# Kernel optimization log

Measured on AMD Instinct MI355X. Metric: run time of the kernel, lower is better.

The kernel has to match this reference:

```python
import jax, jax.numpy as jnp
import numpy as np

# Model dims
T0 = 2048      # tokens (batch*seq flattened)
D = 2048       # hidden_size
E = 256        # n_routed_experts
K = 8          # num_experts_per_tok
G = 8          # expert groups
EG = 32        # experts per group
R = 64         # tucker rank
I = 1408       # moe_intermediate_size


def setup_inputs() -> dict:
    key = jax.random.key(0)
    ks = jax.random.split(key, 12)
    f = lambda k, s: jax.random.normal(k, s, dtype=jnp.float32) * 0.02
    return {
        "hidden_states": jax.random.normal(ks[0], (T0, D), dtype=jnp.float32),
        "w_gate": f(ks[1], (D, E)),
        # Tucker factors per group: shared in-factor A, per-expert core C, shared out-factor B
        "A_gate": f(ks[2], (G, D, R)), "C_gate": f(ks[3], (G, EG, R, R)), "B_gate": f(ks[4], (G, R, I)),
        "A_up":   f(ks[5], (G, D, R)), "C_up":   f(ks[6], (G, EG, R, R)), "B_up":   f(ks[7], (G, R, I)),
        "A_down": f(ks[8], (G, I, R)), "C_down": f(ks[9], (G, EG, R, R)), "B_down": f(ks[10], (G, R, D)),
    }


def _tucker(x, A, C, B, inner):
    # x: [T, d_in], A: [d_in, R], C: [EG, R, R] gathered per-token, B: [R, d_out]
    h1 = x @ A                                    # [T, R]
    h2 = jnp.einsum('tr,trs->ts', h1, C[inner])   # per-token expert core
    return h2 @ B                                 # [T, d_out]


def reference(hidden_states, w_gate, A_gate, C_gate, B_gate,
              A_up, C_up, B_up, A_down, C_down, B_down):
    # Router: softmax in fp32, top-k, renormalize
    logits = hidden_states @ w_gate                              # [T0, E]
    probs = jax.nn.softmax(logits.astype(jnp.float32), axis=-1)
    rw, sel = jax.lax.top_k(probs, K)                            # [T0, K]
    rw = (rw / rw.sum(axis=-1, keepdims=True)).astype(hidden_states.dtype)

    idx = sel.reshape(-1)          # [T0*K] expert ids of dispatched rows
    gid = idx // EG                # group id
    inner = idx % EG               # expert within group
    x = jnp.repeat(hidden_states, K, axis=0)   # repeat_interleave dispatch [T0*K, D]

    out = jnp.zeros_like(x)
    for g in range(G):             # static loop over 8 structurally distinct groups
        m = (gid == g)[:, None]
        xg = jnp.where(m, x, 0.0)  # masked dispatch (zeros flow to zero through the MLP)
        go = _tucker(xg, A_gate[g], C_gate[g], B_gate[g], inner)
        uo = _tucker(xg, A_up[g],   C_up[g],   B_up[g],   inner)
        inter = jax.nn.silu(go) * uo
        do = _tucker(inter, A_down[g], C_down[g], B_down[g], inner)
        out = out + jnp.where(m, do, 0.0)

    # weighted combine
    return (out.reshape(T0, K, D) * rw[..., None]).sum(axis=1)
```

## Files before the change

### kernel.cpp

```cpp
#include <hip/hip_runtime.h>
#include <math.h>

constexpr int T0n = 2048;
constexpr int Dn  = 2048;
constexpr int En  = 256;
constexpr int Gn  = 8;
constexpr int EGn = 32;
constexpr int Rn  = 64;
constexpr int In  = 1408;

constexpr int NROWS = T0n * 8;
constexpr int SEGCAP = NROWS;
constexpr int KSPLIT = 8;

typedef __attribute__((ext_vector_type(8))) short s8v;
typedef __attribute__((ext_vector_type(4))) float f4v;
#define MFMA16(a, b, c) __builtin_amdgcn_mfma_f32_16x16x32_bf16(a, b, c, 0, 0, 0)

__device__ __forceinline__ unsigned short f2bf(float x) {
  unsigned int u = __float_as_uint(x);
  unsigned int r = (u + 0x7FFFu + ((u >> 16) & 1u)) >> 16;
  return (unsigned short)r;
}

struct TD { const float* src; unsigned short* dst; int rows, cols, nbx, per_batch, base; };
struct TD9 { TD t[9]; };

__global__ __launch_bounds__(256) void k_tcvt9(TD9 D) {
  __shared__ float tbuf[32][33];
  int id = blockIdx.x;
  int ti = 0;
#pragma unroll
  for (int i = 1; i < 9; ++i) ti = (id >= D.t[i].base) ? i : ti;
  TD d = D.t[ti];
  int local = id - d.base;
  int bz = local / d.per_batch;
  int rem = local - bz * d.per_batch;
  int by = rem / d.nbx;
  int bx = rem - by * d.nbx;

  size_t boff = (size_t)bz * d.rows * d.cols;
  const float* src = d.src + boff;
  unsigned short* dst = d.dst + boff;
  int c0 = bx * 32, r0 = by * 32;
  int tx = threadIdx.x & 31, ty = threadIdx.x >> 5;
  for (int i = ty; i < 32; i += 8)
    tbuf[i][tx] = src[(size_t)(r0 + i) * d.cols + c0 + tx];
  __syncthreads();
  for (int i = ty; i < 32; i += 8)
    dst[(size_t)(c0 + i) * d.rows + r0 + tx] = f2bf(tbuf[tx][i]);
}

__global__ __launch_bounds__(256) void k_router_part(
    const float* __restrict__ A, const float* __restrict__ B,
    double* __restrict__ part) {
  __shared__ float As[32][68];
  __shared__ float Bs[32][68];
  const int m0 = blockIdx.y * 64, n0 = blockIdx.x * 64;
  const int kc = blockIdx.z;
  const int kbeg = kc * (Dn / KSPLIT);
  const int tid = threadIdx.x;
  const int ty = tid >> 4, tx = tid & 15;
  const int lm = tid & 63, lk8 = (tid >> 6) * 8;
  const int br = tid >> 3, bc = (tid & 7) * 8;

  double acc[4][4] = {};

  for (int k0 = kbeg; k0 < kbeg + Dn / KSPLIT; k0 += 32) {
    float4 a0 = *(const float4*)&A[(size_t)(m0 + lm) * Dn + k0 + lk8];
    float4 a1 = *(const float4*)&A[(size_t)(m0 + lm) * Dn + k0 + lk8 + 4];
    As[lk8 + 0][lm] = a0.x; As[lk8 + 1][lm] = a0.y;
    As[lk8 + 2][lm] = a0.z; As[lk8 + 3][lm] = a0.w;
    As[lk8 + 4][lm] = a1.x; As[lk8 + 5][lm] = a1.y;
    As[lk8 + 6][lm] = a1.z; As[lk8 + 7][lm] = a1.w;
    *(float4*)&Bs[br][bc]     = *(const float4*)&B[(size_t)(k0 + br) * En + n0 + bc];
    *(float4*)&Bs[br][bc + 4] = *(const float4*)&B[(size_t)(k0 + br) * En + n0 + bc + 4];
    __syncthreads();
#pragma unroll
    for (int kk = 0; kk < 32; ++kk) {
      float4 af = *(const float4*)&As[kk][ty * 4];
      float4 bf = *(const float4*)&Bs[kk][tx * 4];
      double a[4] = {(double)af.x, (double)af.y, (double)af.z, (double)af.w};
      double b[4] = {(double)bf.x, (double)bf.y, (double)bf.z, (double)bf.w};
#pragma unroll
      for (int i = 0; i < 4; ++i)
#pragma unroll
        for (int j = 0; j < 4; ++j)
          acc[i][j] += a[i] * b[j];
    }
    __syncthreads();
  }
  double* prow = part + (size_t)kc * T0n * En;
#pragma unroll
  for (int i = 0; i < 4; ++i) {
    int row = m0 + ty * 4 + i;
#pragma unroll
    for (int j2 = 0; j2 < 2; ++j2) {
      double2 dv;
      dv.x = acc[i][j2 * 2 + 0];
      dv.y = acc[i][j2 * 2 + 1];
      *(double2*)&prow[(size_t)row * En + n0 + tx * 4 + j2 * 2] = dv;
    }
  }
}

__global__ __launch_bounds__(256) void k_topk(
    const double* __restrict__ part, int* __restrict__ sel,
    float* __restrict__ rw, int* __restrict__ cnt_e) {
  const int wid = threadIdx.x >> 6, ln = threadIdx.x & 63;
  const int t = blockIdx.x * 4 + wid;

  double v[4];
#pragma unroll
  for (int j = 0; j < 4; ++j) {
    double s = 0.0;
#pragma unroll
    for (int kc = 0; kc < KSPLIT; ++kc)
      s += part[((size_t)kc * T0n + t) * En + ln + 64 * j];
    v[j] = s;
  }

  float topv[8];
  int topi[8];
#pragma unroll
  for (int k = 0; k < 8; ++k) {
    double bv = v[0]; int bi = ln;
#pragma unroll
    for (int j = 1; j < 4; ++j) {
      int cand = ln + 64 * j;
      if (v[j] > bv || (v[j] == bv && cand < bi)) { bv = v[j]; bi = cand; }
    }
#pragma unroll
    for (int off = 32; off > 0; off >>= 1) {
      double ov = __shfl_xor(bv, off);
      int oi = __shfl_xor(bi, off);
      if (ov > bv || (ov == bv && oi < bi)) { bv = ov; bi = oi; }
    }
    topv[k] = (float)bv; topi[k] = bi;
    if ((bi & 63) == ln) v[bi >> 6] = -1e300;
  }

  if (ln < 8) {
    float m = topv[0];
    float ssum = 0.f;
#pragma unroll
    for (int k = 0; k < 8; ++k) ssum += expf(topv[k] - m);
    rw[t * 8 + ln] = expf(topv[ln] - m) / ssum;
    sel[t * 8 + ln] = topi[ln];
    atomicAdd(&cnt_e[topi[ln]], 1);
  }
}

__global__ __launch_bounds__(256) void k_scan(
    const int* __restrict__ cnt_e, int* __restrict__ off_e,
    int* __restrict__ cur_e, int* __restrict__ grp_n) {
  __shared__ int c[256];
  int tid = threadIdx.x;
  c[tid] = cnt_e[tid];
  __syncthreads();
  int g = tid >> 5, ei = tid & 31;
  int run = 0;
  for (int i = 0; i < ei; ++i) run += c[(g << 5) + i];
  off_e[tid] = g * SEGCAP + run;
  cur_e[tid] = g * SEGCAP + run;
  if (ei == 31) grp_n[g] = run + c[tid];
}

__global__ void k_scatter(const int* __restrict__ sel, int* __restrict__ cur_e,
                          int* __restrict__ rseg) {
  int i = blockIdx.x * 256 + threadIdx.x;
  int e = sel[i];
  int pos = atomicAdd(&cur_e[e], 1);
  rseg[pos] = i;
}

__global__ __launch_bounds__(512) void k_h1_mfma(
    const float* __restrict__ H,
    const unsigned short* __restrict__ AgT, const unsigned short* __restrict__ AuT,
    unsigned short* __restrict__ h1gb, unsigned short* __restrict__ h1ub) {
  const int t0 = blockIdx.x * 64;
  const int g = blockIdx.y;
  const unsigned short* Wg = AgT + (size_t)g * Rn * Dn;
  const unsigned short* Wu = AuT + (size_t)g * Rn * Dn;

  __shared__ unsigned short As[64 * 72];
  __shared__ unsigned short Bg_l[64 * 72];
  __shared__ unsigned short Bu_l[64 * 72];
  const int tid = threadIdx.x;
  const int w = tid >> 6, ln = tid & 63;
  const int path = w >> 2, ws = w & 3;
  const int quad = ln >> 4, lane16 = ln & 15;
  const int j = tid >> 3, q = (tid & 7) * 8;

  f4v S[4] = {};

  for (int k0 = 0; k0 < Dn; k0 += 64) {
    {
      float4 v0 = *(const float4*)&H[(size_t)(t0 + j) * Dn + k0 + q];
      float4 v1 = *(const float4*)&H[(size_t)(t0 + j) * Dn + k0 + q + 4];
      ushort4 o0, o1;
      o0.x = f2bf(v0.x); o0.y = f2bf(v0.y); o0.z = f2bf(v0.z); o0.w = f2bf(v0.w);
      o1.x = f2bf(v1.x); o1.y = f2bf(v1.y); o1.z = f2bf(v1.z); o1.w = f2bf(v1.w);
      *(ushort4*)&As[j * 72 + q] = o0;
      *(ushort4*)&As[j * 72 + q + 4] = o1;
      *(uint4*)&Bg_l[j * 72 + q] = *(const uint4*)&Wg[(size_t)j * Dn + k0 + q];
      *(uint4*)&Bu_l[j * 72 + q] = *(const uint4*)&Wu[(size_t)j * Dn + k0 + q];
    }
    __syncthreads();
    const unsigned short* Bl = path ? Bu_l : Bg_l;
#pragma unroll
    for (int kk = 0; kk < 2; ++kk) {
      s8v a = *(const s8v*)&As[(ws * 16 + lane16) * 72 + kk * 32 + quad * 8];
#pragma unroll
      for (int nt = 0; nt < 4; ++nt) {
        s8v b = *(const s8v*)&Bl[(nt * 16 + lane16) * 72 + kk * 32 + quad * 8];
        S[nt] = MFMA16(a, b, S[nt]);
      }
    }
    __syncthreads();
  }
  unsigned short* out = path ? h1ub : h1gb;
#pragma unroll
  for (int nt = 0; nt < 4; ++nt)
#pragma unroll
    for (int r = 0; r < 4; ++r) {
      int row = t0 + ws * 16 + quad * 4 + r;
      int col = g * 64 + nt * 16 + lane16;
      out[(size_t)row * (Gn * Rn) + col] = f2bf(S[nt][r]);
    }
}

__global__ __launch_bounds__(512) void k_core_gu(
    const unsigned short* __restrict__ h1gb, const unsigned short* __restrict__ h1ub,
    const unsigned short* __restrict__ CgT, const unsigned short* __restrict__ CuT,
    const int* __restrict__ rseg, const int* __restrict__ off_e,
    const int* __restrict__ cnt_e,
    unsigned short* __restrict__ h2gb, unsigned short* __restrict__ h2ub) {
  const int e = blockIdx.x;
  const int ne = cnt_e[e];
  if (ne == 0) return;
  const int g = e >> 5;
  const int base = off_e[e];
  __shared__ unsigned short Cg_l[64 * 72];
  __shared__ unsigned short Cu_l[64 * 72];
  __shared__ unsigned short Ags[64 * 72];
  __shared__ unsigned short Aus[64 * 72];
  __shared__ int rids[64];
  const int tid = threadIdx.x;
  const int w = tid >> 6, ln = tid & 63;
  const int path = w >> 2, ws = w & 3;
  const int quad = ln >> 4, lane16 = ln & 15;
  const int j = tid >> 3, q = (tid & 7) * 8;
  {
    const unsigned short* cg = CgT + (size_t)e * (Rn * Rn);
    const unsigned short* cu = CuT + (size_t)e * (Rn * Rn);
    *(uint4*)&Cg_l[j * 72 + q] = *(const uint4*)&cg[j * 64 + q];
    *(uint4*)&Cu_l[j * 72 + q] = *(const uint4*)&cu[j * 64 + q];
  }
  const int ntile = (ne + 63) >> 6;
  for (int it = 0; it < ntile; ++it) {
    int mi = it * 64 + j;
    int rid = (mi < ne) ? rseg[base + mi] : -1;
    if ((tid & 7) == 0) rids[j] = rid;
    uint4 zg = {0, 0, 0, 0}, zu = {0, 0, 0, 0};
    if (rid >= 0) {
      zg = *(const uint4*)&h1gb[(size_t)(rid >> 3) * (Gn * Rn) + g * 64 + q];
      zu = *(const uint4*)&h1ub[(size_t)(rid >> 3) * (Gn * Rn) + g * 64 + q];
    }
    *(uint4*)&Ags[j * 72 + q] = zg;
    *(uint4*)&Aus[j * 72 + q] = zu;
    __syncthreads();
    const unsigned short* Al = path ? Aus : Ags;
    const unsigned short* Cl = path ? Cu_l : Cg_l;
    f4v S[4] = {};
#pragma unroll
    for (int kk = 0; kk < 2; ++kk) {
      s8v a = *(const s8v*)&Al[(ws * 16 + lane16) * 72 + kk * 32 + quad * 8];
#pragma unroll
      for (int nt = 0; nt < 4; ++nt) {
        s8v b = *(const s8v*)&Cl[(nt * 16 + lane16) * 72 + kk * 32 + quad * 8];
        S[nt] = MFMA16(a, b, S[nt]);
      }
    }
    unsigned short* out = path ? h2ub : h2gb;
#pragma unroll
    for (int nt = 0; nt < 4; ++nt)
#pragma unroll
      for (int r = 0; r < 4; ++r) {
        int rid2 = rids[ws * 16 + quad * 4 + r];
        if (rid2 >= 0)
          out[(size_t)rid2 * 64 + nt * 16 + lane16] = f2bf(S[nt][r]);
      }
    __syncthreads();
  }
}

__global__ __launch_bounds__(256) void k_expand_mfma(
    const unsigned short* __restrict__ h2gb, const unsigned short* __restrict__ h2ub,
    const unsigned short* __restrict__ BgT, const unsigned short* __restrict__ BuT,
    const unsigned short* __restrict__ AdT,
    const int* __restrict__ rseg, const int* __restrict__ grp_n,
    float* __restrict__ h1d) {
  const int g = blockIdx.z;
  const int ng = grp_n[g];
  const int m0 = blockIdx.y * 128;
  if (m0 >= ng) return;
  const int c_beg = blockIdx.x * 6;
  const int c_end = min(22, c_beg + 6);

  __shared__ unsigned short Hg_l[128 * 72];
  __shared__ unsigned short Hu_l[128 * 72];
  __shared__ unsigned short Bg_l[64 * 72];
  __shared__ unsigned short Bu_l[64 * 72];
  __shared__ unsigned short Ad_l[64 * 72];
  __shared__ int rids[128];

  const int tid = threadIdx.x;
  const int w = tid >> 6, ln = tid & 63;
  const int quad = ln >> 4, lane16 = ln & 15;

  if (tid < 128) rids[tid] = (m0 + tid < ng) ? rseg[g * SEGCAP + m0 + tid] : -1;
  __syncthreads();
#pragma unroll
  for (int i = 0; i < 4; ++i) {
    int c = tid + i * 256;
    int row = c >> 3, cc = (c & 7) * 8;
    int rid = rids[row];
    uint4 zg = {0, 0, 0, 0}, zu = {0, 0, 0, 0};
    if (rid >= 0) {
      zg = *(const uint4*)&h2gb[(size_t)rid * 64 + cc];
      zu = *(const uint4*)&h2ub[(size_t)rid * 64 + cc];
    }
    *(uint4*)&Hg_l[row * 72 + cc] = zg;
    *(uint4*)&Hu_l[row * 72 + cc] = zu;
  }

  const unsigned short* Bg_base = BgT + (size_t)g * In * Rn;
  const unsigned short* Bu_base = BuT + (size_t)g * In * Rn;
  const unsigned short* Ad_base = AdT + (size_t)g * Rn * In;

  f4v P[2][4] = {};

  for (int c = c_beg; c < c_end; ++c) {
    const int i0 = c * 64;
#pragma unroll
    for (int i = 0; i < 2; ++i) {
      int cq = tid + i * 256;
      int row = cq >> 3, co = (cq & 7) * 8;
      *(uint4*)&Bg_l[row * 72 + co] = *(const uint4*)&Bg_base[(size_t)(i0 + row) * Rn + co];
      *(uint4*)&Bu_l[row * 72 + co] = *(const uint4*)&Bu_base[(size_t)(i0 + row) * Rn + co];
      *(uint4*)&Ad_l[row * 72 + co] = *(const uint4*)&Ad_base[(size_t)row * In + i0 + co];
    }
    __syncthreads();

    f4v Sg[2][4] = {}, Su[2][4] = {};
#pragma unroll
    for (int kk = 0; kk < 2; ++kk) {
      s8v ag[2], au[2], bg[4], bu[4];
#pragma unroll
      for (int mt = 0; mt < 2; ++mt) {
        ag[mt] = *(const s8v*)&Hg_l[(w * 32 + mt * 16 + lane16) * 72 + kk * 32 + quad * 8];
        au[mt] = *(const s8v*)&Hu_l[(w * 32 + mt * 16 + lane16) * 72 + kk * 32 + quad * 8];
      }
#pragma unroll
      for (int nt = 0; nt < 4; ++nt) {
        bg[nt] = *(const s8v*)&Bg_l[(nt * 16 + lane16) * 72 + kk * 32 + quad * 8];
        bu[nt] = *(const s8v*)&Bu_l[(nt * 16 + lane16) * 72 + kk * 32 + quad * 8];
      }
#pragma unroll
      for (int mt = 0; mt < 2; ++mt)
#pragma unroll
        for (int nt = 0; nt < 4; ++nt) {
          Sg[mt][nt] = MFMA16(ag[mt], bg[nt], Sg[mt][nt]);
          Su[mt][nt] = MFMA16(au[mt], bu[nt], Su[mt][nt]);
        }
    }
    __syncthreads();
    {
      unsigned short* ibuf = (w < 2) ? Bg_l : Bu_l;
#pragma unroll
      for (int mt = 0; mt < 2; ++mt)
#pragma unroll
        for (int nt = 0; nt < 4; ++nt)
#pragma unroll
          for (int r = 0; r < 4; ++r) {
            float sg = Sg[mt][nt][r];
            float v = sg / (1.f + __expf(-sg)) * Su[mt][nt][r];
            int row = (w * 32 + mt * 16 + quad * 4 + r) & 63;
            ibuf[row * 72 + nt * 16 + lane16] = f2bf(v);
          }
    }
    __syncthreads();
#pragma unroll
    for (int kk = 0; kk < 2; ++kk) {
      s8v ai[2], bd[4];
#pragma unroll
      for (int mt = 0; mt < 2; ++mt) {
        const unsigned short* src = (w < 2) ? Bg_l : Bu_l;
        int arow = (w * 32 + mt * 16 + lane16) & 63;
        ai[mt] = *(const s8v*)&src[arow * 72 + kk * 32 + quad * 8];
      }
#pragma unroll
      for (int nt = 0; nt < 4; ++nt)
        bd[nt] = *(const s8v*)&Ad_l[(nt * 16 + lane16) * 72 + kk * 32 + quad * 8];
#pragma unroll
      for (int mt = 0; mt < 2; ++mt)
#pragma unroll
        for (int nt = 0; nt < 4; ++nt)
          P[mt][nt] = MFMA16(ai[mt], bd[nt], P[mt][nt]);
    }
    __syncthreads();
  }

#pragma unroll
  for (int mt = 0; mt < 2; ++mt)
#pragma unroll
    for (int nt = 0; nt < 4; ++nt)
#pragma unroll
      for (int r = 0; r < 4; ++r) {
        int lrow = w * 32 + mt * 16 + quad * 4 + r;
        int rid = rids[lrow];
        if (rid >= 0)
          atomicAdd(&h1d[(size_t)rid * 64 + nt * 16 + lane16], P[mt][nt][r]);
      }
}

__global__ __launch_bounds__(512) void k_core_down(
    const float* __restrict__ h1d, const unsigned short* __restrict__ CdT,
    const float* __restrict__ rw,
    const int* __restrict__ rseg, const int* __restrict__ off_e,
    const int* __restrict__ cnt_e,
    float* __restrict__ y) {
  const int e = blockIdx.x;
  const int ne = cnt_e[e];
  if (ne == 0) return;
  const int g = e >> 5;
  const int base = off_e[e];
  __shared__ unsigned short Bd_l[64 * 72];
  __shared__ unsigned short Ad_l[128 * 72];
  __shared__ int rids[128];
  const int tid = threadIdx.x;
  const int w = tid >> 6, ln = tid & 63;
  const int quad = ln >> 4, lane16 = ln & 15;
  {
    int j = tid >> 3, q = (tid & 7) * 8;
    const unsigned short* cd = CdT + (size_t)e * (Rn * Rn);
    *(uint4*)&Bd_l[j * 72 + q] = *(const uint4*)&cd[j * 64 + q];
  }
  const int gj = tid >> 2, gq = (tid & 3) * 16;
  const int ntile = (ne + 127) >> 7;
  for (int it = 0; it < ntile; ++it) {
    int mi = it * 128 + gj;
    int rid = (mi < ne) ? rseg[base + mi] : -1;
    if ((tid & 3) == 0) rids[gj] = rid;
#pragma unroll
    for (int i = 0; i < 4; ++i) {
      int kb = gq + i * 4;
      float4 vd = {0.f, 0.f, 0.f, 0.f};
      if (rid >= 0) vd = *(const float4*)&h1d[(size_t)rid * 64 + kb];
      ushort4 od;
      od.x = f2bf(vd.x); od.y = f2bf(vd.y); od.z = f2bf(vd.z); od.w = f2bf(vd.w);
      *(ushort4*)&Ad_l[gj * 72 + kb] = od;
    }
    __syncthreads();
    f4v Sd[4] = {};
#pragma unroll
    for (int kk = 0; kk < 2; ++kk) {
      s8v ad = *(const s8v*)&Ad_l[(w * 16 + lane16) * 72 + kk * 32 + quad * 8];
#pragma unroll
      for (int nt = 0; nt < 4; ++nt) {
        s8v bd = *(const s8v*)&Bd_l[(nt * 16 + lane16) * 72 + kk * 32 + quad * 8];
        Sd[nt] = MFMA16(ad, bd, Sd[nt]);
      }
    }
#pragma unroll
    for (int nt = 0; nt < 4; ++nt)
#pragma unroll
      for (int r = 0; r < 4; ++r) {
        int rid2 = rids[w * 16 + quad * 4 + r];
        if (rid2 >= 0) {
          float wgt = rw[rid2];
          atomicAdd(&y[(size_t)(rid2 >> 3) * (Gn * Rn) + g * 64 + nt * 16 + lane16],
                    wgt * Sd[nt][r]);
        }
      }
    __syncthreads();
  }
}

__global__ __launch_bounds__(256) void k_combine(
    const float* __restrict__ y, const unsigned short* __restrict__ BdT,
    float* __restrict__ outp) {
  const int t0 = blockIdx.y * 128, n0 = blockIdx.x * 128;
  __shared__ unsigned short As[128 * 72];
  __shared__ unsigned short Bs[128 * 72];
  const int tid = threadIdx.x;
  const int w = tid >> 6, ln = tid & 63;
  const int quad = ln >> 4, lane16 = ln & 15;
  const int mbase = (w >> 1) * 64, nbase = (w & 1) * 64;

  f4v acc[4][4] = {};

  for (int k0 = 0; k0 < Gn * Rn; k0 += 64) {
#pragma unroll
    for (int i = 0; i < 8; ++i) {
      int c = tid + i * 256;
      int row = c >> 4, cc = (c & 15) * 4;
      float4 v = *(const float4*)&y[(size_t)(t0 + row) * (Gn * Rn) + k0 + cc];
      ushort4 o;
      o.x = f2bf(v.x); o.y = f2bf(v.y); o.z = f2bf(v.z); o.w = f2bf(v.w);
      *(ushort4*)&As[row * 72 + cc] = o;
    }
#pragma unroll
    for (int i = 0; i < 4; ++i) {
      int c = tid + i * 256;
      int row = c >> 3, cc = (c & 7) * 8;
      *(uint4*)&Bs[row * 72 + cc] = *(const uint4*)&BdT[(size_t)(n0 + row) * (Gn * Rn) + k0 + cc];
    }
    __syncthreads();
#pragma unroll
    for (int kk = 0; kk < 2; ++kk) {
      s8v a[4], b[4];
#pragma unroll
      for (int mt = 0; mt < 4; ++mt)
        a[mt] = *(const s8v*)&As[(mbase + mt * 16 + lane16) * 72 + kk * 32 + quad * 8];
#pragma unroll
      for (int nt = 0; nt < 4; ++nt)
        b[nt] = *(const s8v*)&Bs[(nbase + nt * 16 + lane16) * 72 + kk * 32 + quad * 8];
#pragma unroll
      for (int mt = 0; mt < 4; ++mt)
#pragma unroll
        for (int nt = 0; nt < 4; ++nt)
          acc[mt][nt] = MFMA16(a[mt], b[nt], acc[mt][nt]);
    }
    __syncthreads();
  }
#pragma unroll
  for (int mt = 0; mt < 4; ++mt)
#pragma unroll
    for (int nt = 0; nt < 4; ++nt)
#pragma unroll
      for (int r = 0; r < 4; ++r)
        outp[(size_t)(t0 + mbase + mt * 16 + quad * 4 + r) * Dn +
             n0 + nbase + nt * 16 + lane16] = acc[mt][nt][r];
}

extern "C" void kernel_launch(void* const* d_in, const int* in_sizes, int n_in,
                              void* d_out, int out_size, void* d_ws, size_t ws_size,
                              hipStream_t stream) {
  const float* hidden = (const float*)d_in[0];
  const float* w_gate = (const float*)d_in[1];
  const float* A_gate = (const float*)d_in[2];
  const float* C_gate = (const float*)d_in[3];
  const float* B_gate = (const float*)d_in[4];
  const float* A_up   = (const float*)d_in[5];
  const float* C_up   = (const float*)d_in[6];
  const float* B_up   = (const float*)d_in[7];
  const float* A_down = (const float*)d_in[8];
  const float* C_down = (const float*)d_in[9];
  const float* B_down = (const float*)d_in[10];
  float* out = (float*)d_out;

  char* base = (char*)d_ws;
  double* part = (double*)d_ws;
  size_t o = 0;
  unsigned short* h2gb = (unsigned short*)(base + o); o += (size_t)NROWS * Rn * 2;
  unsigned short* h2ub = (unsigned short*)(base + o); o += (size_t)NROWS * Rn * 2;
  unsigned short* AgT  = (unsigned short*)(base + o); o += (size_t)Gn * Rn * Dn * 2;
  unsigned short* AuT  = (unsigned short*)(base + o); o += (size_t)Gn * Rn * Dn * 2;
  unsigned short* BgT  = (unsigned short*)(base + o); o += (size_t)Gn * In * Rn * 2;
  unsigned short* BuT  = (unsigned short*)(base + o); o += (size_t)Gn * In * Rn * 2;
  unsigned short* AdT  = (unsigned short*)(base + o); o += (size_t)Gn * Rn * In * 2;
  unsigned short* BdT  = (unsigned short*)(base + o); o += (size_t)Dn * Gn * Rn * 2;
  unsigned short* CgT  = (unsigned short*)(base + o); o += (size_t)En * Rn * Rn * 2;
  unsigned short* CuT  = (unsigned short*)(base + o); o += (size_t)En * Rn * Rn * 2;
  unsigned short* CdT  = (unsigned short*)(base + o); o += (size_t)En * Rn * Rn * 2;
  unsigned short* h1gb = (unsigned short*)(base + o); o += (size_t)T0n * Gn * Rn * 2;
  unsigned short* h1ub = (unsigned short*)(base + o); o += (size_t)T0n * Gn * Rn * 2;
  float* h1d = (float*)(base + o); o += (size_t)NROWS * Rn * 4;
  float* y   = (float*)(base + o); o += (size_t)T0n * Gn * Rn * 4;
  float* rwp = (float*)(base + o); o += (size_t)NROWS * 4;
  int* sel   = (int*)(base + o); o += (size_t)NROWS * 4;
  int* rseg  = (int*)(base + o); o += (size_t)Gn * SEGCAP * 4;
  int* cnt_e = (int*)(base + o); o += En * 4;
  int* off_e = (int*)(base + o); o += En * 4;
  int* cur_e = (int*)(base + o); o += En * 4;
  int* grp_n = (int*)(base + o); o += Gn * 4;

  hipMemsetAsync(cnt_e, 0, En * sizeof(int), stream);

  k_router_part<<<dim3(En / 64, T0n / 64, KSPLIT), 256, 0, stream>>>(
      hidden, w_gate, part);
  k_topk<<<T0n / 4, 256, 0, stream>>>(part, sel, rwp, cnt_e);
  k_scan<<<1, 256, 0, stream>>>(cnt_e, off_e, cur_e, grp_n);
  k_scatter<<<NROWS / 256, 256, 0, stream>>>(sel, cur_e, rseg);

  hipMemsetAsync(h1d, 0, (size_t)NROWS * Rn * sizeof(float), stream);
  hipMemsetAsync(y,   0, (size_t)T0n * Gn * Rn * sizeof(float), stream);

  {
    TD9 D;
    D.t[0] = {A_gate, AgT, Dn, Rn, Rn / 32, (Rn / 32) * (Dn / 32), 0};
    D.t[1] = {A_up,   AuT, Dn, Rn, Rn / 32, (Rn / 32) * (Dn / 32), 1024};
    D.t[2] = {B_gate, BgT, Rn, In, In / 32, (In / 32) * (Rn / 32), 2048};
    D.t[3] = {B_up,   BuT, Rn, In, In / 32, (In / 32) * (Rn / 32), 2752};
    D.t[4] = {A_down, AdT, In, Rn, Rn / 32, (Rn / 32) * (In / 32), 3456};
    D.t[5] = {B_down, BdT, Gn * Rn, Dn, Dn / 32, (Dn / 32) * (Gn * Rn / 32), 4160};
    D.t[6] = {C_gate, CgT, Rn, Rn, 2, 4, 5184};
    D.t[7] = {C_up,   CuT, Rn, Rn, 2, 4, 6208};
    D.t[8] = {C_down, CdT, Rn, Rn, 2, 4, 7232};
    k_tcvt9<<<8256, 256, 0, stream>>>(D);
  }

  k_h1_mfma<<<dim3(T0n / 64, Gn), 512, 0, stream>>>(hidden, AgT, AuT, h1gb, h1ub);
  k_core_gu<<<En, 512, 0, stream>>>(h1gb, h1ub, CgT, CuT,
                                    rseg, off_e, cnt_e, h2gb, h2ub);
  k_expand_mfma<<<dim3(4, NROWS / 128, Gn), 256, 0, stream>>>(
      h2gb, h2ub, BgT, BuT, AdT, rseg, grp_n, h1d);
  k_core_down<<<En, 512, 0, stream>>>(h1d, CdT, rwp,
                                      rseg, off_e, cnt_e, y);
  k_combine<<<dim3(Dn / 128, T0n / 128), 256, 0, stream>>>(y, BdT, out);
}
```

Measured before the change: 339.6 us.

## Fuse hidden bf16 conversion into router, load C cores directly, merge memsets

The router GEMM now stages operands as doubles in LDS and writes a bf16 copy of hidden states from the x==0 column blocks, so k_h1_mfma reads bf16 directly and no longer converts fp32 per group. KSPLIT drops from 8 to 4, halving partial-sum traffic while cutting router parallelism. The per-expert C core matrices are converted and transposed inside the core kernels instead of in the transpose kernel, and the two memsets are merged into one. The costs are larger LDS use in the router, strided LDS writes for the C transposes, and an extra bf16 write of hidden states.

```diff
diff --git a/kernel.cpp b/kernel.cpp
--- a/kernel.cpp
+++ b/kernel.cpp
@@ -11,7 +11,7 @@
 
 constexpr int NROWS = T0n * 8;
 constexpr int SEGCAP = NROWS;
-constexpr int KSPLIT = 8;
+constexpr int KSPLIT = 4;
 
 typedef __attribute__((ext_vector_type(8))) short s8v;
 typedef __attribute__((ext_vector_type(4))) float f4v;
@@ -24,14 +24,14 @@
 }
 
 struct TD { const float* src; unsigned short* dst; int rows, cols, nbx, per_batch, base; };
-struct TD9 { TD t[9]; };
-
-__global__ __launch_bounds__(256) void k_tcvt9(TD9 D) {
+struct TD6 { TD t[6]; };
+
+__global__ __launch_bounds__(256) void k_tcvt6(TD6 D) {
   __shared__ float tbuf[32][33];
   int id = blockIdx.x;
   int ti = 0;
 #pragma unroll
-  for (int i = 1; i < 9; ++i) ti = (id >= D.t[i].base) ? i : ti;
+  for (int i = 1; i < 6; ++i) ti = (id >= D.t[i].base) ? i : ti;
   TD d = D.t[ti];
   int local = id - d.base;
   int bz = local / d.per_batch;
@@ -53,35 +53,47 @@
 
 __global__ __launch_bounds__(256) void k_router_part(
     const float* __restrict__ A, const float* __restrict__ B,
-    double* __restrict__ part) {
-  __shared__ float As[32][68];
-  __shared__ float Bs[32][68];
+    double* __restrict__ part, unsigned short* __restrict__ Hb) {
+  __shared__ double Asd[32][66];
+  __shared__ double Bsd[32][66];
   const int m0 = blockIdx.y * 64, n0 = blockIdx.x * 64;
-  const int kc = blockIdx.z;
-  const int kbeg = kc * (Dn / KSPLIT);
+  const int kbeg = blockIdx.z * (Dn / KSPLIT);
   const int tid = threadIdx.x;
   const int ty = tid >> 4, tx = tid & 15;
   const int lm = tid & 63, lk8 = (tid >> 6) * 8;
   const int br = tid >> 3, bc = (tid & 7) * 8;
+  const bool emitH = (blockIdx.x == 0);
 
   double acc[4][4] = {};
 
   for (int k0 = kbeg; k0 < kbeg + Dn / KSPLIT; k0 += 32) {
     float4 a0 = *(const float4*)&A[(size_t)(m0 + lm) * Dn + k0 + lk8];
     float4 a1 = *(const float4*)&A[(size_t)(m0 + lm) * Dn + k0 + lk8 + 4];
-    As[lk8 + 0][lm] = a0.x; As[lk8 + 1][lm] = a0.y;
-    As[lk8 + 2][lm] = a0.z; As[lk8 + 3][lm] = a0.w;
-    As[lk8 + 4][lm] = a1.x; As[lk8 + 5][lm] = a1.y;
-    As[lk8 + 6][lm] = a1.z; As[lk8 + 7][lm] = a1.w;
-    *(float4*)&Bs[br][bc]     = *(const float4*)&B[(size_t)(k0 + br) * En + n0 + bc];
-    *(float4*)&Bs[br][bc + 4] = *(const float4*)&B[(size_t)(k0 + br) * En + n0 + bc + 4];
+    Asd[lk8 + 0][lm] = (double)a0.x; Asd[lk8 + 1][lm] = (double)a0.y;
+    Asd[lk8 + 2][lm] = (double)a0.z; Asd[lk8 + 3][lm] = (double)a0.w;
+    Asd[lk8 + 4][lm] = (double)a1.x; Asd[lk8 + 5][lm] = (double)a1.y;
+    Asd[lk8 + 6][lm] = (double)a1.z; Asd[lk8 + 7][lm] = (double)a1.w;
+    if (emitH) {
+      ushort4 o0, o1;
+      o0.x = f2bf(a0.x); o0.y = f2bf(a0.y); o0.z = f2bf(a0.z); o0.w = f2bf(a0.w);
+      o1.x = f2bf(a1.x); o1.y = f2bf(a1.y); o1.z = f2bf(a1.z); o1.w = f2bf(a1.w);
+      *(ushort4*)&Hb[(size_t)(m0 + lm) * Dn + k0 + lk8] = o0;
+      *(ushort4*)&Hb[(size_t)(m0 + lm) * Dn + k0 + lk8 + 4] = o1;
+    }
+    float4 b0 = *(const float4*)&B[(size_t)(k0 + br) * En + n0 + bc];
+    float4 b1 = *(const float4*)&B[(size_t)(k0 + br) * En + n0 + bc + 4];
+    Bsd[br][bc + 0] = (double)b0.x; Bsd[br][bc + 1] = (double)b0.y;
+    Bsd[br][bc + 2] = (double)b0.z; Bsd[br][bc + 3] = (double)b0.w;
+    Bsd[br][bc + 4] = (double)b1.x; Bsd[br][bc + 5] = (double)b1.y;
+    Bsd[br][bc + 6] = (double)b1.z; Bsd[br][bc + 7] = (double)b1.w;
     __syncthreads();
 #pragma unroll
     for (int kk = 0; kk < 32; ++kk) {
-      float4 af = *(const float4*)&As[kk][ty * 4];
-      float4 bf = *(const float4*)&Bs[kk][tx * 4];
-      double a[4] = {(double)af.x, (double)af.y, (double)af.z, (double)af.w};
-      double b[4] = {(double)bf.x, (double)bf.y, (double)bf.z, (double)bf.w};
+      double a[4], b[4];
+#pragma unroll
+      for (int i = 0; i < 4; ++i) a[i] = Asd[kk][ty + 16 * i];
+#pragma unroll
+      for (int j = 0; j < 4; ++j) b[j] = Bsd[kk][tx + 16 * j];
 #pragma unroll
       for (int i = 0; i < 4; ++i)
 #pragma unroll
@@ -90,17 +102,13 @@
     }
     __syncthreads();
   }
-  double* prow = part + (size_t)kc * T0n * En;
+  double* prow = part + (size_t)blockIdx.z * T0n * En;
 #pragma unroll
   for (int i = 0; i < 4; ++i) {
-    int row = m0 + ty * 4 + i;
-#pragma unroll
-    for (int j2 = 0; j2 < 2; ++j2) {
-      double2 dv;
-      dv.x = acc[i][j2 * 2 + 0];
-      dv.y = acc[i][j2 * 2 + 1];
-      *(double2*)&prow[(size_t)row * En + n0 + tx * 4 + j2 * 2] = dv;
-    }
+    int row = m0 + ty + 16 * i;
+#pragma unroll
+    for (int j = 0; j < 4; ++j)
+      prow[(size_t)row * En + n0 + tx + 16 * j] = acc[i][j];
   }
 }
 
@@ -175,7 +183,7 @@
 }
 
 __global__ __launch_bounds__(512) void k_h1_mfma(
-    const float* __restrict__ H,
+    const unsigned short* __restrict__ Hb,
     const unsigned short* __restrict__ AgT, const unsigned short* __restrict__ AuT,
     unsigned short* __restrict__ h1gb, unsigned short* __restrict__ h1ub) {
   const int t0 = blockIdx.x * 64;
@@ -195,17 +203,9 @@
   f4v S[4] = {};
 
   for (int k0 = 0; k0 < Dn; k0 += 64) {
-    {
-      float4 v0 = *(const float4*)&H[(size_t)(t0 + j) * Dn + k0 + q];
-      float4 v1 = *(const float4*)&H[(size_t)(t0 + j) * Dn + k0 + q + 4];
-      ushort4 o0, o1;
-      o0.x = f2bf(v0.x); o0.y = f2bf(v0.y); o0.z = f2bf(v0.z); o0.w = f2bf(v0.w);
-      o1.x = f2bf(v1.x); o1.y = f2bf(v1.y); o1.z = f2bf(v1.z); o1.w = f2bf(v1.w);
-      *(ushort4*)&As[j * 72 + q] = o0;
-      *(ushort4*)&As[j * 72 + q + 4] = o1;
-      *(uint4*)&Bg_l[j * 72 + q] = *(const uint4*)&Wg[(size_t)j * Dn + k0 + q];
-      *(uint4*)&Bu_l[j * 72 + q] = *(const uint4*)&Wu[(size_t)j * Dn + k0 + q];
-    }
+    *(uint4*)&As[j * 72 + q]   = *(const uint4*)&Hb[(size_t)(t0 + j) * Dn + k0 + q];
+    *(uint4*)&Bg_l[j * 72 + q] = *(const uint4*)&Wg[(size_t)j * Dn + k0 + q];
+    *(uint4*)&Bu_l[j * 72 + q] = *(const uint4*)&Wu[(size_t)j * Dn + k0 + q];
     __syncthreads();
     const unsigned short* Bl = path ? Bu_l : Bg_l;
 #pragma unroll
@@ -232,7 +232,7 @@
 
 __global__ __launch_bounds__(512) void k_core_gu(
     const unsigned short* __restrict__ h1gb, const unsigned short* __restrict__ h1ub,
-    const unsigned short* __restrict__ CgT, const unsigned short* __restrict__ CuT,
+    const float* __restrict__ Cgate, const float* __restrict__ Cup,
     const int* __restrict__ rseg, const int* __restrict__ off_e,
     const int* __restrict__ cnt_e,
     unsigned short* __restrict__ h2gb, unsigned short* __restrict__ h2ub) {
@@ -252,10 +252,20 @@
   const int quad = ln >> 4, lane16 = ln & 15;
   const int j = tid >> 3, q = (tid & 7) * 8;
   {
-    const unsigned short* cg = CgT + (size_t)e * (Rn * Rn);
-    const unsigned short* cu = CuT + (size_t)e * (Rn * Rn);
-    *(uint4*)&Cg_l[j * 72 + q] = *(const uint4*)&cg[j * 64 + q];
-    *(uint4*)&Cu_l[j * 72 + q] = *(const uint4*)&cu[j * 64 + q];
+    const float* cg = Cgate + (size_t)e * (Rn * Rn);
+    const float* cu = Cup   + (size_t)e * (Rn * Rn);
+    float4 g0 = *(const float4*)&cg[j * 64 + q];
+    float4 g1 = *(const float4*)&cg[j * 64 + q + 4];
+    float4 u0 = *(const float4*)&cu[j * 64 + q];
+    float4 u1 = *(const float4*)&cu[j * 64 + q + 4];
+    Cg_l[(q + 0) * 72 + j] = f2bf(g0.x); Cg_l[(q + 1) * 72 + j] = f2bf(g0.y);
+    Cg_l[(q + 2) * 72 + j] = f2bf(g0.z); Cg_l[(q + 3) * 72 + j] = f2bf(g0.w);
+    Cg_l[(q + 4) * 72 + j] = f2bf(g1.x); Cg_l[(q + 5) * 72 + j] = f2bf(g1.y);
+    Cg_l[(q + 6) * 72 + j] = f2bf(g1.z); Cg_l[(q + 7) * 72 + j] = f2bf(g1.w);
+    Cu_l[(q + 0) * 72 + j] = f2bf(u0.x); Cu_l[(q + 1) * 72 + j] = f2bf(u0.y);
+    Cu_l[(q + 2) * 72 + j] = f2bf(u0.z); Cu_l[(q + 3) * 72 + j] = f2bf(u0.w);
+    Cu_l[(q + 4) * 72 + j] = f2bf(u1.x); Cu_l[(q + 5) * 72 + j] = f2bf(u1.y);
+    Cu_l[(q + 6) * 72 + j] = f2bf(u1.z); Cu_l[(q + 7) * 72 + j] = f2bf(u1.w);
   }
   const int ntile = (ne + 63) >> 6;
   for (int it = 0; it < ntile; ++it) {
@@ -426,7 +436,7 @@
 }
 
 __global__ __launch_bounds__(512) void k_core_down(
-    const float* __restrict__ h1d, const unsigned short* __restrict__ CdT,
+    const float* __restrict__ h1d, const float* __restrict__ Cdown,
     const float* __restrict__ rw,
     const int* __restrict__ rseg, const int* __restrict__ off_e,
     const int* __restrict__ cnt_e,
@@ -444,8 +454,13 @@
   const int quad = ln >> 4, lane16 = ln & 15;
   {
     int j = tid >> 3, q = (tid & 7) * 8;
-    const unsigned short* cd = CdT + (size_t)e * (Rn * Rn);
-    *(uint4*)&Bd_l[j * 72 + q] = *(const uint4*)&cd[j * 64 + q];
+    const float* cd = Cdown + (size_t)e * (Rn * Rn);
+    float4 d0 = *(const float4*)&cd[j * 64 + q];
+    float4 d1 = *(const float4*)&cd[j * 64 + q + 4];
+    Bd_l[(q + 0) * 72 + j] = f2bf(d0.x); Bd_l[(q + 1) * 72 + j] = f2bf(d0.y);
+    Bd_l[(q + 2) * 72 + j] = f2bf(d0.z); Bd_l[(q + 3) * 72 + j] = f2bf(d0.w);
+    Bd_l[(q + 4) * 72 + j] = f2bf(d1.x); Bd_l[(q + 5) * 72 + j] = f2bf(d1.y);
+    Bd_l[(q + 6) * 72 + j] = f2bf(d1.z); Bd_l[(q + 7) * 72 + j] = f2bf(d1.w);
   }
   const int gj = tid >> 2, gq = (tid & 3) * 16;
   const int ntile = (ne + 127) >> 7;
@@ -566,19 +581,17 @@
   size_t o = 0;
   unsigned short* h2gb = (unsigned short*)(base + o); o += (size_t)NROWS * Rn * 2;
   unsigned short* h2ub = (unsigned short*)(base + o); o += (size_t)NROWS * Rn * 2;
-  unsigned short* AgT  = (unsigned short*)(base + o); o += (size_t)Gn * Rn * Dn * 2;
-  unsigned short* AuT  = (unsigned short*)(base + o); o += (size_t)Gn * Rn * Dn * 2;
-  unsigned short* BgT  = (unsigned short*)(base + o); o += (size_t)Gn * In * Rn * 2;
-  unsigned short* BuT  = (unsigned short*)(base + o); o += (size_t)Gn * In * Rn * 2;
-  unsigned short* AdT  = (unsigned short*)(base + o); o += (size_t)Gn * Rn * In * 2;
-  unsigned short* BdT  = (unsigned short*)(base + o); o += (size_t)Dn * Gn * Rn * 2;
-  unsigned short* CgT  = (unsigned short*)(base + o); o += (size_t)En * Rn * Rn * 2;
-  unsigned short* CuT  = (unsigned short*)(base + o); o += (size_t)En * Rn * Rn * 2;
-  unsigned short* CdT  = (unsigned short*)(base + o); o += (size_t)En * Rn * Rn * 2;
   unsigned short* h1gb = (unsigned short*)(base + o); o += (size_t)T0n * Gn * Rn * 2;
   unsigned short* h1ub = (unsigned short*)(base + o); o += (size_t)T0n * Gn * Rn * 2;
   float* h1d = (float*)(base + o); o += (size_t)NROWS * Rn * 4;
   float* y   = (float*)(base + o); o += (size_t)T0n * Gn * Rn * 4;
+  unsigned short* Hb  = (unsigned short*)(base + o); o += (size_t)T0n * Dn * 2;
+  unsigned short* AgT = (unsigned short*)(base + o); o += (size_t)Gn * Rn * Dn * 2;
+  unsigned short* AuT = (unsigned short*)(base + o); o += (size_t)Gn * Rn * Dn * 2;
+  unsigned short* BgT = (unsigned short*)(base + o); o += (size_t)Gn * In * Rn * 2;
+  unsigned short* BuT = (unsigned short*)(base + o); o += (size_t)Gn * In * Rn * 2;
+  unsigned short* AdT = (unsigned short*)(base + o); o += (size_t)Gn * Rn * In * 2;
+  unsigned short* BdT = (unsigned short*)(base + o); o += (size_t)Dn * Gn * Rn * 2;
   float* rwp = (float*)(base + o); o += (size_t)NROWS * 4;
   int* sel   = (int*)(base + o); o += (size_t)NROWS * 4;
   int* rseg  = (int*)(base + o); o += (size_t)Gn * SEGCAP * 4;
@@ -590,34 +603,30 @@
   hipMemsetAsync(cnt_e, 0, En * sizeof(int), stream);
 
   k_router_part<<<dim3(En / 64, T0n / 64, KSPLIT), 256, 0, stream>>>(
-      hidden, w_gate, part);
+      hidden, w_gate, part, Hb);
   k_topk<<<T0n / 4, 256, 0, stream>>>(part, sel, rwp, cnt_e);
   k_scan<<<1, 256, 0, stream>>>(cnt_e, off_e, cur_e, grp_n);
   k_scatter<<<NROWS / 256, 256, 0, stream>>>(sel, cur_e, rseg);
 
-  hipMemsetAsync(h1d, 0, (size_t)NROWS * Rn * sizeof(float), stream);
-  hipMemsetAsync(y,   0, (size_t)T0n * Gn * Rn * sizeof(float), stream);
+  hipMemsetAsync(h1d, 0, (size_t)(NROWS * Rn + T0n * Gn * Rn) * sizeof(float), stream);
 
   {
-    TD9 D;
+    TD6 D;
     D.t[0] = {A_gate, AgT, Dn, Rn, Rn / 32, (Rn / 32) * (Dn / 32), 0};
     D.t[1] = {A_up,   AuT, Dn, Rn, Rn / 32, (Rn / 32) * (Dn / 32), 1024};
     D.t[2] = {B_gate, BgT, Rn, In, In / 32, (In / 32) * (Rn / 32), 2048};
     D.t[3] = {B_up,   BuT, Rn, In, In / 32, (In / 32) * (Rn / 32), 2752};
     D.t[4] = {A_down, AdT, In, Rn, Rn / 32, (Rn / 32) * (In / 32), 3456};
     D.t[5] = {B_down, BdT, Gn * Rn, Dn, Dn / 32, (Dn / 32) * (Gn * Rn / 32), 4160};
-    D.t[6] = {C_gate, CgT, Rn, Rn, 2, 4, 5184};
-    D.t[7] = {C_up,   CuT, Rn, Rn, 2, 4, 6208};
-    D.t[8] = {C_down, CdT, Rn, Rn, 2, 4, 7232};
-    k_tcvt9<<<8256, 256, 0, stream>>>(D);
-  }
-
-  k_h1_mfma<<<dim3(T0n / 64, Gn), 512, 0, stream>>>(hidden, AgT, AuT, h1gb, h1ub);
-  k_core_gu<<<En, 512, 0, stream>>>(h1gb, h1ub, CgT, CuT,
+    k_tcvt6<<<5184, 256, 0, stream>>>(D);
+  }
+
+  k_h1_mfma<<<dim3(T0n / 64, Gn), 512, 0, stream>>>(Hb, AgT, AuT, h1gb, h1ub);
+  k_core_gu<<<En, 512, 0, stream>>>(h1gb, h1ub, C_gate, C_up,
                                     rseg, off_e, cnt_e, h2gb, h2ub);
   k_expand_mfma<<<dim3(4, NROWS / 128, Gn), 256, 0, stream>>>(
       h2gb, h2ub, BgT, BuT, AdT, rseg, grp_n, h1d);
-  k_core_down<<<En, 512, 0, stream>>>(h1d, CdT, rwp,
+  k_core_down<<<En, 512, 0, stream>>>(h1d, C_down, rwp,
                                       rseg, off_e, cnt_e, y);
   k_combine<<<dim3(Dn / 128, T0n / 128), 256, 0, stream>>>(y, BdT, out);
 }
```

Measured after the change: 354.3 us. 4.3% more time.
